# Performance work log

Measured on AMD Instinct MI355X. Metric: run time of the kernel, lower is better.

The kernel has to match this reference:

```python
import jax, jax.numpy as jnp
import numpy as np

B, T, D, H = 4096, 16, 512, 8
DH = D // H
EPS = 1e-5

def _layer_norm(x, w, b):
    mu = jnp.mean(x, axis=-1, keepdims=True)
    var = jnp.mean(jnp.square(x - mu), axis=-1, keepdims=True)
    return (x - mu) * jax.lax.rsqrt(var + EPS) * w + b

def setup_inputs() -> dict:
    key = jax.random.key(0)
    ks = jax.random.split(key, 12)
    inp = {
        'structural_output': jax.random.normal(ks[0], (B, T, D), jnp.float32),
        'position_embedding_clustering_coefficient': jax.random.normal(ks[1], (B, T, D), jnp.float32),
        'position_embedding_bidirectional_links_ratio': jax.random.normal(ks[2], (B, T, D), jnp.float32),
        'exist_nodes': jax.random.randint(ks[3], (B, T), 0, 2, jnp.int32),
        'pos_emb': jax.random.normal(ks[4], (T, D), jnp.float32) * 0.02,
        'Qw': jax.random.normal(ks[5], (D, D), jnp.float32) / np.sqrt(D),
        'Kw': jax.random.normal(ks[6], (D, D), jnp.float32) / np.sqrt(D),
        'Vw': jax.random.normal(ks[7], (D, D), jnp.float32) / np.sqrt(D),
        'ln_w': jnp.ones((D,), jnp.float32),
        'ln_b': jnp.zeros((D,), jnp.float32),
        'ff1_w': jax.random.normal(ks[8], (D, D), jnp.float32) / np.sqrt(D),
        'ff1_b': jnp.zeros((D,), jnp.float32),
        'prelu_a': jnp.array(0.25, jnp.float32),
        'ff2_w': jax.random.normal(ks[9], (2, D), jnp.float32) / np.sqrt(D),
        'ff2_b': jnp.zeros((2,), jnp.float32),
    }
    return inp

def reference(structural_output, position_embedding_clustering_coefficient,
              position_embedding_bidirectional_links_ratio, exist_nodes,
              pos_emb, Qw, Kw, Vw, ln_w, ln_b, ff1_w, ff1_b, prelu_a, ff2_w, ff2_b):
    x = structural_output
    # temporal input = x + positional embeddings, then shared LayerNorm
    t_in = _layer_norm(
        x + pos_emb[None, :, :]
        + position_embedding_clustering_coefficient
        + position_embedding_bidirectional_links_ratio,
        ln_w, ln_b)
    # fused-style QKV projections, split into heads [B,T,H,DH]
    q = (t_in @ Qw).reshape(B, T, H, DH)
    k = (t_in @ Kw).reshape(B, T, H, DH)
    v = (t_in @ Vw).reshape(B, T, H, DH)
    scores = jnp.einsum('bihd,bjhd->bhij', q, k) / np.sqrt(DH)  # [B,H,T,T]
    causal = jnp.tril(jnp.ones((T, T), bool))
    scores = jnp.where(causal[None, None], scores, jnp.float32(-1e9))
    attn = jax.nn.softmax(scores, axis=-1)  # dropout is identity at inference
    out = jnp.einsum('bhij,bjhd->bihd', attn, v).reshape(B, T, D)
    # residual with pre-norm input, shared LayerNorm again
    y = _layer_norm(out + x, ln_w, ln_b)
    # feed forward: Linear(D,D) -> PReLU -> Linear(D,2)
    h = y @ ff1_w.T + ff1_b
    h = jnp.maximum(h, 0) + prelu_a * jnp.minimum(h, 0)
    return h @ ff2_w.T + ff2_b
```

## Files before the change

### kernel.cpp

```cpp
#include <hip/hip_runtime.h>

#define NROWS 65536
#define DD 512
#define EPS_LN 1e-5f

typedef __bf16 bfx8 __attribute__((ext_vector_type(8)));
typedef float fx4 __attribute__((ext_vector_type(4)));

__device__ __forceinline__ unsigned short f2bf(float f) {
  unsigned int u = __builtin_bit_cast(unsigned int, f);
  u += 0x7fffu + ((u >> 16) & 1u);
  return (unsigned short)(u >> 16);
}
__device__ __forceinline__ float bflo(unsigned int u) { return __builtin_bit_cast(float, u << 16); }
__device__ __forceinline__ float bfhi(unsigned int u) { return __builtin_bit_cast(float, u & 0xffff0000u); }
__device__ __forceinline__ unsigned int pack2(float a, float b) {
  return (unsigned int)f2bf(a) | ((unsigned int)f2bf(b) << 16);
}
__device__ __forceinline__ float wave_sum(float v) {
  #pragma unroll
  for (int off = 32; off; off >>= 1) v += __shfl_xor(v, off);
  return v;
}

__global__ __launch_bounds__(256) void prep_weights(
    const float* __restrict__ Qw, const float* __restrict__ Kw, const float* __restrict__ Vw,
    const float* __restrict__ ff1w, unsigned short* __restrict__ WqkvT, unsigned short* __restrict__ W1T) {
  int idx = blockIdx.x * 256 + threadIdx.x;
  if (idx < 1536 * 512) {
    int j = idx >> 9, k = idx & 511;
    const float* src = (j < 512) ? Qw : (j < 1024 ? Kw : Vw);
    WqkvT[idx] = f2bf(src[k * 512 + (j & 511)]);
  } else {
    int i2 = idx - 1536 * 512;
    W1T[i2] = f2bf(ff1w[i2]);
  }
}

__global__ __launch_bounds__(256) void ln1_kernel(
    const float* __restrict__ x, const float* __restrict__ pcc, const float* __restrict__ pblr,
    const float* __restrict__ pos, const float* __restrict__ lnw, const float* __restrict__ lnb,
    unsigned short* __restrict__ t_in) {
  int row = blockIdx.x * 4 + (threadIdx.x >> 6);
  int lane = threadIdx.x & 63;
  size_t base = (size_t)row * DD + lane * 8;
  int t = row & 15;
  const fx4* x4 = (const fx4*)(x + base);
  const fx4* p4 = (const fx4*)(pcc + base);
  const fx4* q4 = (const fx4*)(pblr + base);
  const fx4* e4 = (const fx4*)(pos + t * DD + lane * 8);
  fx4 a0 = x4[0], a1 = x4[1], b0 = p4[0], b1 = p4[1], c0 = q4[0], c1 = q4[1], d0 = e4[0], d1 = e4[1];
  float s[8];
  #pragma unroll
  for (int j = 0; j < 4; ++j) { s[j] = a0[j] + b0[j] + c0[j] + d0[j]; s[j+4] = a1[j] + b1[j] + c1[j] + d1[j]; }
  float sum = 0.f;
  #pragma unroll
  for (int j = 0; j < 8; ++j) sum += s[j];
  sum = wave_sum(sum);
  float mu = sum * (1.0f / 512.0f);
  float vs = 0.f;
  #pragma unroll
  for (int j = 0; j < 8; ++j) { float d = s[j] - mu; vs += d * d; }
  vs = wave_sum(vs);
  float rs = rsqrtf(vs * (1.0f / 512.0f) + EPS_LN);
  const fx4* w4 = (const fx4*)(lnw + lane * 8);
  const fx4* bb4 = (const fx4*)(lnb + lane * 8);
  fx4 w0 = w4[0], w1 = w4[1], g0 = bb4[0], g1 = bb4[1];
  float o[8];
  #pragma unroll
  for (int j = 0; j < 4; ++j) { o[j] = (s[j] - mu) * rs * w0[j] + g0[j]; o[j+4] = (s[j+4] - mu) * rs * w1[j] + g1[j]; }
  uint4 pk;
  pk.x = pack2(o[0], o[1]); pk.y = pack2(o[2], o[3]); pk.z = pack2(o[4], o[5]); pk.w = pack2(o[6], o[7]);
  *(uint4*)(t_in + base) = pk;
}

__global__ __launch_bounds__(256) void gemm_bt(
    const unsigned short* __restrict__ A, const unsigned short* __restrict__ BT,
    unsigned short* __restrict__ C, int ldc,
    const float* __restrict__ bias, const float* __restrict__ prelu_a) {
  __shared__ unsigned short As[128 * 72];
  __shared__ unsigned short Bs[128 * 72];
  int tid = threadIdx.x;
  int row0 = blockIdx.x * 128, col0 = blockIdx.y * 128;
  int wid = tid >> 6, lane = tid & 63;
  int wm = (wid >> 1) * 64, wn = (wid & 1) * 64;
  fx4 acc[4][4] = {};
  for (int k0 = 0; k0 < 512; k0 += 64) {
    #pragma unroll
    for (int c = 0; c < 4; ++c) {
      int v = c * 256 + tid;
      int r = v >> 3, kk = (v & 7) * 8;
      uint4 da = *(const uint4*)(A + (size_t)(row0 + r) * 512 + k0 + kk);
      uint4 db = *(const uint4*)(BT + (size_t)(col0 + r) * 512 + k0 + kk);
      *(uint4*)(As + r * 72 + kk) = da;
      *(uint4*)(Bs + r * 72 + kk) = db;
    }
    __syncthreads();
    #pragma unroll
    for (int ks = 0; ks < 2; ++ks) {
      int koff = ks * 32 + (lane >> 4) * 8;
      bfx8 af[4], bf[4];
      #pragma unroll
      for (int m = 0; m < 4; ++m) af[m] = *(const bfx8*)(As + (wm + m * 16 + (lane & 15)) * 72 + koff);
      #pragma unroll
      for (int n = 0; n < 4; ++n) bf[n] = *(const bfx8*)(Bs + (wn + n * 16 + (lane & 15)) * 72 + koff);
      #pragma unroll
      for (int m = 0; m < 4; ++m)
        #pragma unroll
        for (int n = 0; n < 4; ++n)
          acc[m][n] = __builtin_amdgcn_mfma_f32_16x16x32_bf16(af[m], bf[n], acc[m][n], 0, 0, 0);
    }
    __syncthreads();
  }
  bool do_prelu = (prelu_a != nullptr);
  float pa = do_prelu ? *prelu_a : 0.f;
  #pragma unroll
  for (int m = 0; m < 4; ++m) {
    #pragma unroll
    for (int n = 0; n < 4; ++n) {
      int rbase = row0 + wm + m * 16 + ((lane >> 4) * 4);
      int cidx = col0 + wn + n * 16 + (lane & 15);
      float bv = bias ? bias[cidx] : 0.f;
      #pragma unroll
      for (int r = 0; r < 4; ++r) {
        float v = acc[m][n][r] + bv;
        if (do_prelu) v = fmaxf(v, 0.f) + pa * fminf(v, 0.f);
        C[(size_t)(rbase + r) * ldc + cidx] = f2bf(v);
      }
    }
  }
}

__global__ __launch_bounds__(256) void attn_kernel(
    const unsigned short* __restrict__ qkv, unsigned short* __restrict__ attn_out) {
  __shared__ unsigned short q_s[16 * 520];
  __shared__ unsigned short k_s[16 * 520];
  __shared__ unsigned short v_s[16 * 520];
  __shared__ float p_s[8 * 16 * 18];
  int b = blockIdx.x, tid = threadIdx.x;
  #pragma unroll
  for (int c = 0; c < 12; ++c) {
    int v = c * 256 + tid;
    int i = v / 192, colv = v % 192, col = colv * 8;
    uint4 d = *(const uint4*)(qkv + (size_t)(b * 16 + i) * 1536 + col);
    unsigned short* dst = (col < 512) ? (q_s + i * 520 + col)
                        : (col < 1024) ? (k_s + i * 520 + (col - 512))
                                       : (v_s + i * 520 + (col - 1024));
    *(uint4*)dst = d;
  }
  __syncthreads();
  if (tid < 128) {
    int h = tid >> 4, i = tid & 15;
    uint4 qv[8];
    #pragma unroll
    for (int db = 0; db < 8; ++db) qv[db] = *(const uint4*)(q_s + i * 520 + h * 64 + db * 8);
    float sc[16];
    float mx = -3e38f;
    #pragma unroll
    for (int j = 0; j < 16; ++j) {
      float acc = 0.f;
      const unsigned short* kr = k_s + j * 520 + h * 64;
      #pragma unroll
      for (int db = 0; db < 8; ++db) {
        uint4 kv = *(const uint4*)(kr + db * 8);
        acc += bflo(qv[db].x) * bflo(kv.x) + bfhi(qv[db].x) * bfhi(kv.x);
        acc += bflo(qv[db].y) * bflo(kv.y) + bfhi(qv[db].y) * bfhi(kv.y);
        acc += bflo(qv[db].z) * bflo(kv.z) + bfhi(qv[db].z) * bfhi(kv.z);
        acc += bflo(qv[db].w) * bflo(kv.w) + bfhi(qv[db].w) * bfhi(kv.w);
      }
      acc = (j <= i) ? acc * 0.125f : -3e38f;
      sc[j] = acc;
      mx = fmaxf(mx, acc);
    }
    float sum = 0.f;
    #pragma unroll
    for (int j = 0; j < 16; ++j) {
      float e = (j <= i) ? __expf(sc[j] - mx) : 0.f;
      sc[j] = e; sum += e;
    }
    float inv = 1.0f / sum;
    float* prow = p_s + (h * 16 + i) * 18;
    #pragma unroll
    for (int j = 0; j < 16; ++j) prow[j] = sc[j] * inv;
  }
  __syncthreads();
  #pragma unroll
  for (int rep = 0; rep < 4; ++rep) {
    int idx = rep * 256 + tid;
    int i = idx >> 6, cb = idx & 63, col = cb * 8, h = col >> 6;
    const float* prow = p_s + (h * 16 + i) * 18;
    float o[8] = {0, 0, 0, 0, 0, 0, 0, 0};
    #pragma unroll
    for (int j = 0; j < 16; ++j) {
      float p = prow[j];
      uint4 vv = *(const uint4*)(v_s + j * 520 + col);
      o[0] += p * bflo(vv.x); o[1] += p * bfhi(vv.x);
      o[2] += p * bflo(vv.y); o[3] += p * bfhi(vv.y);
      o[4] += p * bflo(vv.z); o[5] += p * bfhi(vv.z);
      o[6] += p * bflo(vv.w); o[7] += p * bfhi(vv.w);
    }
    uint4 pk;
    pk.x = pack2(o[0], o[1]); pk.y = pack2(o[2], o[3]); pk.z = pack2(o[4], o[5]); pk.w = pack2(o[6], o[7]);
    *(uint4*)(attn_out + (size_t)(b * 16 + i) * 512 + col) = pk;
  }
}

__global__ __launch_bounds__(256) void ln2_kernel(
    const unsigned short* __restrict__ attn, const float* __restrict__ x,
    const float* __restrict__ lnw, const float* __restrict__ lnb, unsigned short* __restrict__ y) {
  int row = blockIdx.x * 4 + (threadIdx.x >> 6);
  int lane = threadIdx.x & 63;
  size_t base = (size_t)row * DD + lane * 8;
  uint4 av = *(const uint4*)(attn + base);
  const fx4* x4 = (const fx4*)(x + base);
  fx4 a0 = x4[0], a1 = x4[1];
  float s[8];
  s[0] = bflo(av.x) + a0[0]; s[1] = bfhi(av.x) + a0[1];
  s[2] = bflo(av.y) + a0[2]; s[3] = bfhi(av.y) + a0[3];
  s[4] = bflo(av.z) + a1[0]; s[5] = bfhi(av.z) + a1[1];
  s[6] = bflo(av.w) + a1[2]; s[7] = bfhi(av.w) + a1[3];
  float sum = 0.f;
  #pragma unroll
  for (int j = 0; j < 8; ++j) sum += s[j];
  sum = wave_sum(sum);
  float mu = sum * (1.0f / 512.0f);
  float vs = 0.f;
  #pragma unroll
  for (int j = 0; j < 8; ++j) { float d = s[j] - mu; vs += d * d; }
  vs = wave_sum(vs);
  float rs = rsqrtf(vs * (1.0f / 512.0f) + EPS_LN);
  const fx4* w4 = (const fx4*)(lnw + lane * 8);
  const fx4* bb4 = (const fx4*)(lnb + lane * 8);
  fx4 w0 = w4[0], w1 = w4[1], g0 = bb4[0], g1 = bb4[1];
  float o[8];
  #pragma unroll
  for (int j = 0; j < 4; ++j) { o[j] = (s[j] - mu) * rs * w0[j] + g0[j]; o[j+4] = (s[j+4] - mu) * rs * w1[j] + g1[j]; }
  uint4 pk;
  pk.x = pack2(o[0], o[1]); pk.y = pack2(o[2], o[3]); pk.z = pack2(o[4], o[5]); pk.w = pack2(o[6], o[7]);
  *(uint4*)(y + base) = pk;
}

__global__ __launch_bounds__(256) void ff2_kernel(
    const unsigned short* __restrict__ h, const float* __restrict__ w2,
    const float* __restrict__ b2, float* __restrict__ out) {
  int row = blockIdx.x * 4 + (threadIdx.x >> 6);
  int lane = threadIdx.x & 63;
  size_t base = (size_t)row * DD + lane * 8;
  uint4 hv = *(const uint4*)(h + base);
  float f[8];
  f[0] = bflo(hv.x); f[1] = bfhi(hv.x); f[2] = bflo(hv.y); f[3] = bfhi(hv.y);
  f[4] = bflo(hv.z); f[5] = bfhi(hv.z); f[6] = bflo(hv.w); f[7] = bfhi(hv.w);
  const fx4* w0p = (const fx4*)(w2 + lane * 8);
  const fx4* w1p = (const fx4*)(w2 + 512 + lane * 8);
  fx4 w00 = w0p[0], w01 = w0p[1], w10 = w1p[0], w11 = w1p[1];
  float a0 = 0.f, a1 = 0.f;
  #pragma unroll
  for (int j = 0; j < 4; ++j) {
    a0 += f[j] * w00[j] + f[j+4] * w01[j];
    a1 += f[j] * w10[j] + f[j+4] * w11[j];
  }
  a0 = wave_sum(a0);
  a1 = wave_sum(a1);
  if (lane == 0) {
    out[(size_t)row * 2 + 0] = a0 + b2[0];
    out[(size_t)row * 2 + 1] = a1 + b2[1];
  }
}

extern "C" void kernel_launch(void* const* d_in, const int* in_sizes, int n_in,
                              void* d_out, int out_size, void* d_ws, size_t ws_size,
                              hipStream_t stream) {
  const float* x    = (const float*)d_in[0];
  const float* pcc  = (const float*)d_in[1];
  const float* pblr = (const float*)d_in[2];
  const float* pos  = (const float*)d_in[4];
  const float* Qw   = (const float*)d_in[5];
  const float* Kw   = (const float*)d_in[6];
  const float* Vw   = (const float*)d_in[7];
  const float* lnw  = (const float*)d_in[8];
  const float* lnb  = (const float*)d_in[9];
  const float* ff1w = (const float*)d_in[10];
  const float* ff1b = (const float*)d_in[11];
  const float* pra  = (const float*)d_in[12];
  const float* ff2w = (const float*)d_in[13];
  const float* ff2b = (const float*)d_in[14];
  float* out = (float*)d_out;

  char* ws = (char*)d_ws;
  unsigned short* WqkvT = (unsigned short*)ws;
  unsigned short* W1T   = (unsigned short*)(ws + 1572864);
  unsigned short* t_in  = (unsigned short*)(ws + 2097152);
  unsigned short* qkv   = (unsigned short*)(ws + 2097152 + 67108864);
  unsigned short* attn_o = t_in;
  unsigned short* ybuf  = qkv;
  unsigned short* hbuf  = (unsigned short*)(ws + 2097152 + 67108864 + 67108864);

  prep_weights<<<4096, 256, 0, stream>>>(Qw, Kw, Vw, ff1w, WqkvT, W1T);
  ln1_kernel<<<NROWS / 4, 256, 0, stream>>>(x, pcc, pblr, pos, lnw, lnb, t_in);
  gemm_bt<<<dim3(NROWS / 128, 1536 / 128), 256, 0, stream>>>(t_in, WqkvT, qkv, 1536, nullptr, nullptr);
  attn_kernel<<<4096, 256, 0, stream>>>(qkv, attn_o);
  ln2_kernel<<<NROWS / 4, 256, 0, stream>>>(attn_o, x, lnw, lnb, ybuf);
  gemm_bt<<<dim3(NROWS / 128, 512 / 128), 256, 0, stream>>>(ybuf, W1T, hbuf, 512, ff1b, pra);
  ff2_kernel<<<NROWS / 4, 256, 0, stream>>>(hbuf, ff2w, ff2b, out);
}
```

Measured before the change: 846.8 us.

## Fuse attention with LN2, fold FF2 into GEMM epilogue, use direct LDS loads

```diff
diff --git a/kernel.cpp b/kernel.cpp
--- a/kernel.cpp
+++ b/kernel.cpp
@@ -22,18 +22,28 @@
   for (int off = 32; off; off >>= 1) v += __shfl_xor(v, off);
   return v;
 }
+__device__ __forceinline__ void glds16(const unsigned short* g, unsigned short* l) {
+  __builtin_amdgcn_global_load_lds(
+      (const __attribute__((address_space(1))) unsigned int*)g,
+      (__attribute__((address_space(3))) unsigned int*)l, 16, 0, 0);
+}
 
 __global__ __launch_bounds__(256) void prep_weights(
     const float* __restrict__ Qw, const float* __restrict__ Kw, const float* __restrict__ Vw,
-    const float* __restrict__ ff1w, unsigned short* __restrict__ WqkvT, unsigned short* __restrict__ W1T) {
+    const float* __restrict__ ff1w, const float* __restrict__ b2,
+    unsigned short* __restrict__ WqkvT, unsigned short* __restrict__ W1T,
+    float* __restrict__ out) {
   int idx = blockIdx.x * 256 + threadIdx.x;
   if (idx < 1536 * 512) {
     int j = idx >> 9, k = idx & 511;
     const float* src = (j < 512) ? Qw : (j < 1024 ? Kw : Vw);
     WqkvT[idx] = f2bf(src[k * 512 + (j & 511)]);
-  } else {
+  } else if (idx < 1536 * 512 + 512 * 512) {
     int i2 = idx - 1536 * 512;
     W1T[i2] = f2bf(ff1w[i2]);
+  } else {
+    int i3 = idx - (1536 * 512 + 512 * 512);
+    if (i3 < NROWS * 2) out[i3] = b2[i3 & 1];
   }
 }
 
@@ -74,65 +84,106 @@
   *(uint4*)(t_in + base) = pk;
 }
 
+template<bool FUSE>
 __global__ __launch_bounds__(256) void gemm_bt(
     const unsigned short* __restrict__ A, const unsigned short* __restrict__ BT,
     unsigned short* __restrict__ C, int ldc,
-    const float* __restrict__ bias, const float* __restrict__ prelu_a) {
-  __shared__ unsigned short As[128 * 72];
-  __shared__ unsigned short Bs[128 * 72];
+    const float* __restrict__ bias, const float* __restrict__ prelu_a,
+    const float* __restrict__ w2, float* __restrict__ out) {
+  __shared__ unsigned short As[128 * 64];
+  __shared__ unsigned short Bs[128 * 64];
   int tid = threadIdx.x;
-  int row0 = blockIdx.x * 128, col0 = blockIdx.y * 128;
+  int col0 = blockIdx.x * 128, row0 = blockIdx.y * 128;
   int wid = tid >> 6, lane = tid & 63;
   int wm = (wid >> 1) * 64, wn = (wid & 1) * 64;
+  int srow = (lane >> 3);
+  int skk = (lane & 7) * 8;
   fx4 acc[4][4] = {};
   for (int k0 = 0; k0 < 512; k0 += 64) {
     #pragma unroll
     for (int c = 0; c < 4; ++c) {
-      int v = c * 256 + tid;
-      int r = v >> 3, kk = (v & 7) * 8;
-      uint4 da = *(const uint4*)(A + (size_t)(row0 + r) * 512 + k0 + kk);
-      uint4 db = *(const uint4*)(BT + (size_t)(col0 + r) * 512 + k0 + kk);
-      *(uint4*)(As + r * 72 + kk) = da;
-      *(uint4*)(Bs + r * 72 + kk) = db;
+      int chunk = wid * 4 + c;
+      int r = chunk * 8 + srow;
+      glds16(A + (size_t)(row0 + r) * 512 + k0 + skk, As + chunk * 512);
+      glds16(BT + (size_t)(col0 + r) * 512 + k0 + skk, Bs + chunk * 512);
     }
     __syncthreads();
     #pragma unroll
     for (int ks = 0; ks < 2; ++ks) {
       int koff = ks * 32 + (lane >> 4) * 8;
-      bfx8 af[4], bf[4];
-      #pragma unroll
-      for (int m = 0; m < 4; ++m) af[m] = *(const bfx8*)(As + (wm + m * 16 + (lane & 15)) * 72 + koff);
-      #pragma unroll
-      for (int n = 0; n < 4; ++n) bf[n] = *(const bfx8*)(Bs + (wn + n * 16 + (lane & 15)) * 72 + koff);
+      bfx8 af[4], bfr[4];
+      #pragma unroll
+      for (int m = 0; m < 4; ++m) af[m] = *(const bfx8*)(As + (wm + m * 16 + (lane & 15)) * 64 + koff);
+      #pragma unroll
+      for (int n = 0; n < 4; ++n) bfr[n] = *(const bfx8*)(Bs + (wn + n * 16 + (lane & 15)) * 64 + koff);
       #pragma unroll
       for (int m = 0; m < 4; ++m)
         #pragma unroll
         for (int n = 0; n < 4; ++n)
-          acc[m][n] = __builtin_amdgcn_mfma_f32_16x16x32_bf16(af[m], bf[n], acc[m][n], 0, 0, 0);
+          acc[m][n] = __builtin_amdgcn_mfma_f32_16x16x32_bf16(af[m], bfr[n], acc[m][n], 0, 0, 0);
     }
     __syncthreads();
   }
-  bool do_prelu = (prelu_a != nullptr);
-  float pa = do_prelu ? *prelu_a : 0.f;
-  #pragma unroll
-  for (int m = 0; m < 4; ++m) {
+  int fq = lane >> 4, fr = lane & 15;
+  if constexpr (!FUSE) {
+    #pragma unroll
+    for (int m = 0; m < 4; ++m) {
+      #pragma unroll
+      for (int n = 0; n < 4; ++n) {
+        int rbase = row0 + wm + m * 16 + fq * 4;
+        int cidx = col0 + wn + n * 16 + fr;
+        #pragma unroll
+        for (int r = 0; r < 4; ++r)
+          C[(size_t)(rbase + r) * ldc + cidx] = f2bf(acc[m][n][r]);
+      }
+    }
+  } else {
+    float pa = *prelu_a;
+    float p0[16] = {}, p1[16] = {};
     #pragma unroll
     for (int n = 0; n < 4; ++n) {
-      int rbase = row0 + wm + m * 16 + ((lane >> 4) * 4);
-      int cidx = col0 + wn + n * 16 + (lane & 15);
-      float bv = bias ? bias[cidx] : 0.f;
-      #pragma unroll
-      for (int r = 0; r < 4; ++r) {
-        float v = acc[m][n][r] + bv;
-        if (do_prelu) v = fmaxf(v, 0.f) + pa * fminf(v, 0.f);
-        C[(size_t)(rbase + r) * ldc + cidx] = f2bf(v);
-      }
-    }
-  }
-}
-
-__global__ __launch_bounds__(256) void attn_kernel(
-    const unsigned short* __restrict__ qkv, unsigned short* __restrict__ attn_out) {
+      int cidx = col0 + wn + n * 16 + fr;
+      float bv = bias[cidx];
+      float wa = w2[cidx], wb = w2[512 + cidx];
+      #pragma unroll
+      for (int m = 0; m < 4; ++m) {
+        #pragma unroll
+        for (int r = 0; r < 4; ++r) {
+          float v = acc[m][n][r] + bv;
+          v = fmaxf(v, 0.f) + pa * fminf(v, 0.f);
+          p0[m * 4 + r] += v * wa;
+          p1[m * 4 + r] += v * wb;
+        }
+      }
+    }
+    #pragma unroll
+    for (int off = 1; off < 16; off <<= 1) {
+      #pragma unroll
+      for (int t = 0; t < 16; ++t) {
+        p0[t] += __shfl_xor(p0[t], off);
+        p1[t] += __shfl_xor(p1[t], off);
+      }
+    }
+    if (fr == 0) {
+      #pragma unroll
+      for (int m = 0; m < 4; ++m) {
+        #pragma unroll
+        for (int r = 0; r < 4; ++r) {
+          int row = row0 + wm + m * 16 + fq * 4 + r;
+          __hip_atomic_fetch_add(&out[(size_t)row * 2 + 0], p0[m * 4 + r],
+                                 __ATOMIC_RELAXED, __HIP_MEMORY_SCOPE_AGENT);
+          __hip_atomic_fetch_add(&out[(size_t)row * 2 + 1], p1[m * 4 + r],
+                                 __ATOMIC_RELAXED, __HIP_MEMORY_SCOPE_AGENT);
+        }
+      }
+    }
+  }
+}
+
+__global__ __launch_bounds__(256) void attn_ln2_kernel(
+    const unsigned short* __restrict__ qkv, const float* __restrict__ x,
+    const float* __restrict__ lnw, const float* __restrict__ lnb,
+    unsigned short* __restrict__ y) {
   __shared__ unsigned short q_s[16 * 520];
   __shared__ unsigned short k_s[16 * 520];
   __shared__ unsigned short v_s[16 * 520];
@@ -184,10 +235,11 @@
     for (int j = 0; j < 16; ++j) prow[j] = sc[j] * inv;
   }
   __syncthreads();
+  int lane = tid & 63;
   #pragma unroll
   for (int rep = 0; rep < 4; ++rep) {
-    int idx = rep * 256 + tid;
-    int i = idx >> 6, cb = idx & 63, col = cb * 8, h = col >> 6;
+    int i = rep * 4 + (tid >> 6);
+    int col = lane * 8, h = col >> 6;
     const float* prow = p_s + (h * 16 + i) * 18;
     float o[8] = {0, 0, 0, 0, 0, 0, 0, 0};
     #pragma unroll
@@ -199,71 +251,31 @@
       o[4] += p * bflo(vv.z); o[5] += p * bfhi(vv.z);
       o[6] += p * bflo(vv.w); o[7] += p * bfhi(vv.w);
     }
+    size_t base = (size_t)(b * 16 + i) * 512 + col;
+    const fx4* x4 = (const fx4*)(x + base);
+    fx4 xa = x4[0], xb = x4[1];
+    float s[8];
+    #pragma unroll
+    for (int j = 0; j < 4; ++j) { s[j] = o[j] + xa[j]; s[j+4] = o[j+4] + xb[j]; }
+    float sum = 0.f;
+    #pragma unroll
+    for (int j = 0; j < 8; ++j) sum += s[j];
+    sum = wave_sum(sum);
+    float mu = sum * (1.0f / 512.0f);
+    float vs = 0.f;
+    #pragma unroll
+    for (int j = 0; j < 8; ++j) { float d = s[j] - mu; vs += d * d; }
+    vs = wave_sum(vs);
+    float rs = rsqrtf(vs * (1.0f / 512.0f) + EPS_LN);
+    const fx4* w4 = (const fx4*)(lnw + col);
+    const fx4* bb4 = (const fx4*)(lnb + col);
+    fx4 w0 = w4[0], w1 = w4[1], g0 = bb4[0], g1 = bb4[1];
+    float oo[8];
+    #pragma unroll
+    for (int j = 0; j < 4; ++j) { oo[j] = (s[j] - mu) * rs * w0[j] + g0[j]; oo[j+4] = (s[j+4] - mu) * rs * w1[j] + g1[j]; }
     uint4 pk;
-    pk.x = pack2(o[0], o[1]); pk.y = pack2(o[2], o[3]); pk.z = pack2(o[4], o[5]); pk.w = pack2(o[6], o[7]);
-    *(uint4*)(attn_out + (size_t)(b * 16 + i) * 512 + col) = pk;
-  }
-}
-
-__global__ __launch_bounds__(256) void ln2_kernel(
-    const unsigned short* __restrict__ attn, const float* __restrict__ x,
-    const float* __restrict__ lnw, const float* __restrict__ lnb, unsigned short* __restrict__ y) {
-  int row = blockIdx.x * 4 + (threadIdx.x >> 6);
-  int lane = threadIdx.x & 63;
-  size_t base = (size_t)row * DD + lane * 8;
-  uint4 av = *(const uint4*)(attn + base);
-  const fx4* x4 = (const fx4*)(x + base);
-  fx4 a0 = x4[0], a1 = x4[1];
-  float s[8];
-  s[0] = bflo(av.x) + a0[0]; s[1] = bfhi(av.x) + a0[1];
-  s[2] = bflo(av.y) + a0[2]; s[3] = bfhi(av.y) + a0[3];
-  s[4] = bflo(av.z) + a1[0]; s[5] = bfhi(av.z) + a1[1];
-  s[6] = bflo(av.w) + a1[2]; s[7] = bfhi(av.w) + a1[3];
-  float sum = 0.f;
-  #pragma unroll
-  for (int j = 0; j < 8; ++j) sum += s[j];
-  sum = wave_sum(sum);
-  float mu = sum * (1.0f / 512.0f);
-  float vs = 0.f;
-  #pragma unroll
-  for (int j = 0; j < 8; ++j) { float d = s[j] - mu; vs += d * d; }
-  vs = wave_sum(vs);
-  float rs = rsqrtf(vs * (1.0f / 512.0f) + EPS_LN);
-  const fx4* w4 = (const fx4*)(lnw + lane * 8);
-  const fx4* bb4 = (const fx4*)(lnb + lane * 8);
-  fx4 w0 = w4[0], w1 = w4[1], g0 = bb4[0], g1 = bb4[1];
-  float o[8];
-  #pragma unroll
-  for (int j = 0; j < 4; ++j) { o[j] = (s[j] - mu) * rs * w0[j] + g0[j]; o[j+4] = (s[j+4] - mu) * rs * w1[j] + g1[j]; }
-  uint4 pk;
-  pk.x = pack2(o[0], o[1]); pk.y = pack2(o[2], o[3]); pk.z = pack2(o[4], o[5]); pk.w = pack2(o[6], o[7]);
-  *(uint4*)(y + base) = pk;
-}
-
-__global__ __launch_bounds__(256) void ff2_kernel(
-    const unsigned short* __restrict__ h, const float* __restrict__ w2,
-    const float* __restrict__ b2, float* __restrict__ out) {
-  int row = blockIdx.x * 4 + (threadIdx.x >> 6);
-  int lane = threadIdx.x & 63;
-  size_t base = (size_t)row * DD + lane * 8;
-  uint4 hv = *(const uint4*)(h + base);
-  float f[8];
-  f[0] = bflo(hv.x); f[1] = bfhi(hv.x); f[2] = bflo(hv.y); f[3] = bfhi(hv.y);
-  f[4] = bflo(hv.z); f[5] = bfhi(hv.z); f[6] = bflo(hv.w); f[7] = bfhi(hv.w);
-  const fx4* w0p = (const fx4*)(w2 + lane * 8);
-  const fx4* w1p = (const fx4*)(w2 + 512 + lane * 8);
-  fx4 w00 = w0p[0], w01 = w0p[1], w10 = w1p[0], w11 = w1p[1];
-  float a0 = 0.f, a1 = 0.f;
-  #pragma unroll
-  for (int j = 0; j < 4; ++j) {
-    a0 += f[j] * w00[j] + f[j+4] * w01[j];
-    a1 += f[j] * w10[j] + f[j+4] * w11[j];
-  }
-  a0 = wave_sum(a0);
-  a1 = wave_sum(a1);
-  if (lane == 0) {
-    out[(size_t)row * 2 + 0] = a0 + b2[0];
-    out[(size_t)row * 2 + 1] = a1 + b2[1];
+    pk.x = pack2(oo[0], oo[1]); pk.y = pack2(oo[2], oo[3]); pk.z = pack2(oo[4], oo[5]); pk.w = pack2(oo[6], oo[7]);
+    *(uint4*)(y + base) = pk;
   }
 }
 
@@ -291,15 +303,13 @@
   unsigned short* W1T   = (unsigned short*)(ws + 1572864);
   unsigned short* t_in  = (unsigned short*)(ws + 2097152);
   unsigned short* qkv   = (unsigned short*)(ws + 2097152 + 67108864);
-  unsigned short* attn_o = t_in;
   unsigned short* ybuf  = qkv;
-  unsigned short* hbuf  = (unsigned short*)(ws + 2097152 + 67108864 + 67108864);
-
-  prep_weights<<<4096, 256, 0, stream>>>(Qw, Kw, Vw, ff1w, WqkvT, W1T);
+
+  prep_weights<<<4608, 256, 0, stream>>>(Qw, Kw, Vw, ff1w, ff2b, WqkvT, W1T, out);
   ln1_kernel<<<NROWS / 4, 256, 0, stream>>>(x, pcc, pblr, pos, lnw, lnb, t_in);
-  gemm_bt<<<dim3(NROWS / 128, 1536 / 128), 256, 0, stream>>>(t_in, WqkvT, qkv, 1536, nullptr, nullptr);
-  attn_kernel<<<4096, 256, 0, stream>>>(qkv, attn_o);
-  ln2_kernel<<<NROWS / 4, 256, 0, stream>>>(attn_o, x, lnw, lnb, ybuf);
-  gemm_bt<<<dim3(NROWS / 128, 512 / 128), 256, 0, stream>>>(ybuf, W1T, hbuf, 512, ff1b, pra);
-  ff2_kernel<<<NROWS / 4, 256, 0, stream>>>(hbuf, ff2w, ff2b, out);
-}
+  gemm_bt<false><<<dim3(1536 / 128, NROWS / 128), 256, 0, stream>>>(
+      t_in, WqkvT, qkv, 1536, nullptr, nullptr, nullptr, nullptr);
+  attn_ln2_kernel<<<4096, 256, 0, stream>>>(qkv, x, lnw, lnb, ybuf);
+  gemm_bt<true><<<dim3(512 / 128, NROWS / 128), 256, 0, stream>>>(
+      ybuf, W1T, nullptr, 0, ff1b, pra, ff2w, out);
+}
```

Measured after the change: 808.0 us. 4.6% less time.
